# Kernel optimization log

Hardware: AMD Instinct MI355X
Metric: run time of the kernel (lower is better)

Reference implementation:

```python
import jax, jax.numpy as jnp
import numpy as np

B, T, N, FIN = 32, 12, 1024, 64
K, OUT_F = 3, 64


def setup_inputs() -> dict:
    key = jax.random.key(0)
    k1, k2, k3 = jax.random.split(key, 3)
    x = jax.random.normal(k1, (B, T, N, FIN), dtype=jnp.float32)
    A = jax.random.uniform(k2, (B, N, N), dtype=jnp.float32)
    # Xavier-uniform-like init for Theta [K, in_f, out_f]
    limit = float(np.sqrt(6.0 / (FIN + OUT_F)))
    Theta = jax.random.uniform(k3, (K, FIN, OUT_F), dtype=jnp.float32,
                               minval=-limit, maxval=limit)
    return {"x": x, "A": A, "Theta": Theta}


def reference(x, A, Theta):
    Bb, Tt, Nn, Fin = x.shape
    Kk = Theta.shape[0]
    I = jnp.broadcast_to(jnp.eye(Nn, dtype=x.dtype), (Bb, Nn, Nn))
    # lambda_max = max row-sum of A, clamped to >= 1
    lambda_max = jnp.maximum(jnp.max(jnp.sum(A, axis=-1), axis=-1), 1.0)
    L = 2.0 * A / lambda_max[:, None, None] - I  # scaled Laplacian surrogate [B,N,N]
    out = jnp.zeros((Bb, Tt, Nn, Theta.shape[-1]), dtype=x.dtype)
    T_prev2, T_prev = None, I
    for k in range(Kk):  # small fixed K-hop loop
        if k == 0:
            T_k = I
        elif k == 1:
            T_k = L
        else:
            T_k = 2.0 * jnp.einsum('bnm,bmp->bnp', L, T_prev) - T_prev2
        T_prev2, T_prev = T_prev, T_k
        rhs = jnp.einsum('btnf,fo->btno', x, Theta[k])   # feature transform
        out = out + jnp.einsum('bnm,btmo->btno', T_k, rhs)  # graph aggregation
    return jax.nn.relu(out)
```

## Files before the change

kernel.cpp:

```cpp
#include <hip/hip_runtime.h>

typedef unsigned short ushort_t;
typedef unsigned char uchar_t;
typedef __attribute__((ext_vector_type(8))) __bf16 bf16x8;
typedef __attribute__((ext_vector_type(4))) float f32x4;
typedef __attribute__((ext_vector_type(8))) unsigned short u16x8;
typedef __attribute__((ext_vector_type(8))) int i32x8;

#define NB 32
#define TT 12
#define NNODE 1024
#define FF 64
#define OO 64
#define TO 768

#define SCL_ONE 127
#define SCL_E   118

__device__ __forceinline__ unsigned short f2bf(float f) {
    unsigned u = __float_as_uint(f);
    u += 0x7FFFu + ((u >> 16) & 1u);
    return (unsigned short)(u >> 16);
}
__device__ __forceinline__ float bf2f(unsigned short h) {
    return __uint_as_float(((unsigned)h) << 16);
}
__device__ __forceinline__ unsigned char f2fp8(float f) {
    return (unsigned char)(__builtin_amdgcn_cvt_pk_fp8_f32(f, f, 0, false) & 0xff);
}

__device__ __forceinline__ void gload16(const void* g, void* l) {
    __builtin_amdgcn_global_load_lds(
        (const __attribute__((address_space(1))) unsigned int*)g,
        (__attribute__((address_space(3))) unsigned int*)l, 16, 0, 0);
}

__global__ void k_init(unsigned* lam) {
    if (threadIdx.x < NB) lam[threadIdx.x] = 0x3F800000u;
}

__global__ __launch_bounds__(256) void k_rowmax(const float* __restrict__ A,
                                                unsigned* __restrict__ lam) {
    const int b = blockIdx.x >> 4;
    const int chunk = blockIdx.x & 15;
    const int w = threadIdx.x >> 6, lane = threadIdx.x & 63;
    const float* Ab = A + (size_t)b * NNODE * NNODE;
    float mx = 0.0f;
    for (int r = 0; r < 16; ++r) {
        const float* rp = Ab + (size_t)(chunk * 64 + w * 16 + r) * NNODE;
        float s = 0.0f;
#pragma unroll
        for (int j = 0; j < 16; ++j) s += rp[lane + j * 64];
#pragma unroll
        for (int off = 32; off > 0; off >>= 1) s += __shfl_down(s, off, 64);
        if (lane == 0) mx = fmaxf(mx, s);
    }
    if (lane == 0) atomicMax(&lam[b], __float_as_uint(mx));
}

__global__ __launch_bounds__(256) void k_escale(const float* __restrict__ A,
                                                const unsigned* __restrict__ lam,
                                                uchar_t* __restrict__ E8) {
    const size_t idx = ((size_t)blockIdx.x * 256 + threadIdx.x) * 8;
    const int b = (int)(idx >> 20);
    const float scl = 1024.0f / __uint_as_float(lam[b]);
    const float4 v0 = *(const float4*)(A + idx);
    const float4 v1 = *(const float4*)(A + idx + 4);
    unsigned lo = 0, hi = 0;
    lo = (unsigned)__builtin_amdgcn_cvt_pk_fp8_f32(v0.x * scl, v0.y * scl, (int)lo, false);
    lo = (unsigned)__builtin_amdgcn_cvt_pk_fp8_f32(v0.z * scl, v0.w * scl, (int)lo, true);
    hi = (unsigned)__builtin_amdgcn_cvt_pk_fp8_f32(v1.x * scl, v1.y * scl, (int)hi, false);
    hi = (unsigned)__builtin_amdgcn_cvt_pk_fp8_f32(v1.z * scl, v1.w * scl, (int)hi, true);
    uint2 pk; pk.x = lo; pk.y = hi;
    *(uint2*)(E8 + idx) = pk;
}

__global__ void k_theta(const float* __restrict__ Th, ushort_t* __restrict__ Tht) {
    int tid = blockIdx.x * 256 + threadIdx.x;
    if (tid < 3 * 64 * 64) {
        int k = tid >> 12, rem = tid & 4095, o = rem >> 6, f = rem & 63;
        Tht[tid] = f2bf(Th[(k << 12) + (f << 6) + o]);
    }
}

__global__ __launch_bounds__(512, 5) void k_feature(const float* __restrict__ x,
                                                    const ushort_t* __restrict__ Tht,
                                                    ushort_t* __restrict__ Pb,
                                                    ushort_t* __restrict__ Qc,
                                                    uchar_t* __restrict__ R2f8) {
    __shared__ __align__(16) uchar_t th[3 * 64 * 128];
    __shared__ __align__(16) uchar_t tbuf[26624];
    ushort_t* tbq = (ushort_t*)tbuf;
    char* tbr = (char*)(tbuf + 17408);

    const int n0 = blockIdx.x * 128;
    const int t = blockIdx.y;
    const int b = blockIdx.z;
    const int tid = threadIdx.x;
    const int w = tid >> 6, lane = tid & 63, quad = lane >> 4, l15 = lane & 15;

#pragma unroll
    for (int i = 0; i < 3; ++i) {
        int chunk = i * 512 + tid;
        int ko = chunk >> 3, c = chunk & 7;
        int phys = c ^ (ko & 7);
        const int4 v = *(const int4*)(Tht + ko * 64 + c * 8);
        *(int4*)(th + ko * 128 + phys * 16) = v;
    }

    const float* xr = x + (((size_t)b * TT + t) * NNODE + n0 + w * 16 + l15) * FF;
    bf16x8 af[2];
#pragma unroll
    for (int ks = 0; ks < 2; ++ks) {
        const float4 v0 = *(const float4*)(xr + ks * 32 + quad * 8);
        const float4 v1 = *(const float4*)(xr + ks * 32 + quad * 8 + 4);
        u16x8 p;
        p[0] = f2bf(v0.x); p[1] = f2bf(v0.y); p[2] = f2bf(v0.z); p[3] = f2bf(v0.w);
        p[4] = f2bf(v1.x); p[5] = f2bf(v1.y); p[6] = f2bf(v1.z); p[7] = f2bf(v1.w);
        af[ks] = *(bf16x8*)&p;
    }
    __syncthreads();

    f32x4 acc[3][4];
#pragma unroll
    for (int k = 0; k < 3; ++k)
#pragma unroll
        for (int cb = 0; cb < 4; ++cb) acc[k][cb] = (f32x4){0.f, 0.f, 0.f, 0.f};

#pragma unroll
    for (int k = 0; k < 3; ++k)
#pragma unroll
        for (int ks = 0; ks < 2; ++ks)
#pragma unroll
            for (int cb = 0; cb < 4; ++cb) {
                const int o = cb * 16 + l15;
                const int c = (ks * 4 + quad) ^ (o & 7);
                const bf16x8 bfr = *(const bf16x8*)(th + (k * 64 + o) * 128 + c * 16);
                acc[k][cb] = __builtin_amdgcn_mfma_f32_16x16x32_bf16(af[ks], bfr, acc[k][cb], 0, 0, 0);
            }

    ushort_t* Pbb = Pb + (((size_t)b * TT + t) * NNODE + n0) * OO;
#pragma unroll
    for (int cb = 0; cb < 4; ++cb)
#pragma unroll
        for (int r = 0; r < 4; ++r) {
            const int n = w * 16 + quad * 4 + r;
            const int o = cb * 16 + l15;
            Pbb[(size_t)n * OO + o] = f2bf(acc[0][cb][r] - acc[2][cb][r]);
        }

#pragma unroll
    for (int cb = 0; cb < 4; ++cb)
#pragma unroll
        for (int r = 0; r < 4; ++r) {
            const int nl = w * 16 + quad * 4 + r;
            const int o = cb * 16 + l15;
            tbq[o * 136 + nl] = f2bf(acc[1][cb][r] - 2.0f * acc[2][cb][r]);
            tbr[o * 144 + nl] = (char)f2fp8(acc[2][cb][r]);
        }
    __syncthreads();

    {
        const int o = tid >> 3, seg = tid & 7;
        ushort_t* qrow = Qc + ((size_t)b * TO + t * 64 + o) * NNODE + n0 + seg * 16;
        const ushort_t* sq = tbq + o * 136 + seg * 16;
        *(u16x8*)(qrow) = *(const u16x8*)(sq);
        *(u16x8*)(qrow + 8) = *(const u16x8*)(sq + 8);
        uchar_t* rrow = R2f8 + ((size_t)b * TO + t * 64 + o) * NNODE + n0 + seg * 16;
        *(int4*)rrow = *(const int4*)(tbr + o * 144 + seg * 16);
    }
}

template <int MODE>
__global__ __launch_bounds__(256, 3) void k_gemm8(const uchar_t* __restrict__ Aop, size_t aBS,
                                                  const uchar_t* __restrict__ Bop, size_t bBS,
                                                  const ushort_t* __restrict__ Qc,
                                                  uchar_t* __restrict__ Zf8,
                                                  ushort_t* __restrict__ Pbp,
                                                  float* __restrict__ outp) {
    __shared__ __align__(16) uchar_t smem[49152];
    const int bid = blockIdx.x;
    const int xcd = bid & 7, y = bid >> 3;
    const int tile = y % 48;
    const int b = xcd + 8 * (y / 48);
    const int tm = (MODE == 1) ? (tile >> 3) : (tile / 6);
    const int tn = (MODE == 1) ? (tile & 7) : (tile % 6);
    const int m0 = tm * 128, n0 = tn * 128;
    const int tid = threadIdx.x;
    const int w = tid >> 6, lane = tid & 63, quad = lane >> 4, l15 = lane & 15;
    const int wr = w >> 1, wc = w & 1;
    const uchar_t* Ab = Aop + (size_t)b * aBS + (size_t)m0 * NNODE;
    const uchar_t* Bb = Bop + (size_t)b * bBS + (size_t)n0 * NNODE;

    int ldso[4];
    size_t goff[4];
#pragma unroll
    for (int i = 0; i < 4; ++i) {
        int slot = i * 256 + tid;
        int row = slot >> 3;
        int lc = (slot & 7) ^ (row & 7);
        ldso[i] = slot * 16;
        goff[i] = (size_t)row * NNODE + lc * 16;
    }

    f32x4 acc[4][4];
#pragma unroll
    for (int i = 0; i < 4; ++i)
#pragma unroll
        for (int j = 0; j < 4; ++j) acc[i][j] = (f32x4){0.f, 0.f, 0.f, 0.f};

#pragma unroll
    for (int i = 0; i < 4; ++i) gload16(Ab + goff[i], smem + ldso[i]);
#pragma unroll
    for (int i = 0; i < 4; ++i) gload16(Bb + goff[i], smem + 16384 + ldso[i]);

#pragma unroll
    for (int kk = 0; kk < 8; ++kk) {
        const uchar_t* At = smem;
        const uchar_t* Bt = smem + 16384 + ((kk & 1) << 14);
        uchar_t* Btn = smem + 16384 + (((kk & 1) ^ 1) << 14);
        if (kk < 7) {
            const int k0 = (kk + 1) << 7;
#pragma unroll
            for (int i = 0; i < 4; ++i) gload16(Bb + k0 + goff[i], Btn + ldso[i]);
            asm volatile("s_waitcnt vmcnt(4)" ::: "memory");
        } else {
            asm volatile("s_waitcnt vmcnt(0)" ::: "memory");
        }
        __builtin_amdgcn_s_barrier();

        i32x8 af[4], bfr[4];
#pragma unroll
        for (int i = 0; i < 4; ++i) {
            const int m = wr * 64 + i * 16 + l15;
            const int n = wc * 64 + i * 16 + l15;
            const int4 alo = *(const int4*)(At + m * 128 + (((quad << 1)) ^ (m & 7)) * 16);
            const int4 ahi = *(const int4*)(At + m * 128 + (((quad << 1) | 1) ^ (m & 7)) * 16);
            const int4 blo = *(const int4*)(Bt + n * 128 + (((quad << 1)) ^ (n & 7)) * 16);
            const int4 bhi = *(const int4*)(Bt + n * 128 + (((quad << 1) | 1) ^ (n & 7)) * 16);
            af[i] = (i32x8){alo.x, alo.y, alo.z, alo.w, ahi.x, ahi.y, ahi.z, ahi.w};
            bfr[i] = (i32x8){blo.x, blo.y, blo.z, blo.w, bhi.x, bhi.y, bhi.z, bhi.w};
        }
        asm volatile("s_waitcnt lgkmcnt(0)" ::: "memory");
        __builtin_amdgcn_s_barrier();
        if (kk < 7) {
            const int k0 = (kk + 1) << 7;
#pragma unroll
            for (int i = 0; i < 4; ++i) gload16(Ab + k0 + goff[i], smem + ldso[i]);
        }
        __builtin_amdgcn_s_setprio(1);
#pragma unroll
        for (int i = 0; i < 4; ++i)
#pragma unroll
            for (int j = 0; j < 4; ++j)
                acc[i][j] = __builtin_amdgcn_mfma_scale_f32_16x16x128_f8f6f4(
                    af[i], bfr[j], acc[i][j], 0, 0, 0, SCL_ONE, 0, SCL_E);
        __builtin_amdgcn_s_setprio(0);
    }
    __syncthreads();

    if (MODE == 1) {
        ushort_t* tb = (ushort_t*)smem;
        const ushort_t* Qb = Qc + (size_t)b * TO * NNODE;
        uchar_t* Zb = Zf8 + (size_t)b * TO * NNODE;
#pragma unroll
        for (int i = 0; i < 4; ++i)
#pragma unroll
            for (int r = 0; r < 4; ++r) {
                const int cl = wr * 64 + i * 16 + quad * 4 + r;
                const int c = m0 + cl;
#pragma unroll
                for (int j = 0; j < 4; ++j) {
                    const int nl = wc * 64 + j * 16 + l15;
                    const size_t zi = (size_t)c * NNODE + n0 + nl;
                    const float z = bf2f(Qb[zi]) + 2.0f * acc[i][j][r];
                    Zb[zi] = f2fp8(z);
                    tb[nl * 136 + cl] = f2bf(z);
                }
            }
        __syncthreads();
        const int t0 = m0 >> 6;
        const int row = tid >> 1, half = tid & 1;
        ushort_t* prow = Pbp + (((size_t)b * TT + t0 + half) * NNODE + n0 + row) * OO;
        const ushort_t* srow = tb + row * 136 + half * 64;
#pragma unroll
        for (int s = 0; s < 8; ++s) {
            u16x8 pv = *(const u16x8*)(prow + s * 8);
            u16x8 zv = *(const u16x8*)(srow + s * 8);
            u16x8 rv;
#pragma unroll
            for (int e = 0; e < 8; ++e) rv[e] = f2bf(bf2f(pv[e]) - bf2f(zv[e]));
            *(u16x8*)(prow + s * 8) = rv;
        }
    } else {
#pragma unroll
        for (int i = 0; i < 4; ++i)
#pragma unroll
            for (int r = 0; r < 4; ++r) {
                const int n = m0 + wr * 64 + i * 16 + quad * 4 + r;
#pragma unroll
                for (int j = 0; j < 4; ++j) {
                    const int c = n0 + wc * 64 + j * 16 + l15;
                    const int t = c >> 6, o = c & 63;
                    const size_t id = (((size_t)b * TT + t) * NNODE + n) * OO + o;
                    outp[id] = fmaxf(bf2f(Pbp[id]) + acc[i][j][r], 0.0f);
                }
            }
    }
}

extern "C" void kernel_launch(void* const* d_in, const int* in_sizes, int n_in,
                              void* d_out, int out_size, void* d_ws, size_t ws_size,
                              hipStream_t stream) {
    const float* x = (const float*)d_in[0];
    const float* A = (const float*)d_in[1];
    const float* Th = (const float*)d_in[2];
    float* out = (float*)d_out;
    char* ws = (char*)d_ws;

    unsigned* lam = (unsigned*)ws;
    uchar_t* E8 = (uchar_t*)(ws + 256);
    uchar_t* R2f8 = E8 + (size_t)NB * NNODE * NNODE;
    uchar_t* Zf8 = R2f8 + (size_t)NB * TO * NNODE;
    ushort_t* Qc = (ushort_t*)(Zf8 + (size_t)NB * TO * NNODE);
    ushort_t* Pb = Qc + (size_t)NB * TO * NNODE;
    ushort_t* Tht = Pb + (size_t)NB * TT * NNODE * OO;

    k_init<<<1, 64, 0, stream>>>(lam);
    k_rowmax<<<512, 256, 0, stream>>>(A, lam);
    k_escale<<<16384, 256, 0, stream>>>(A, lam, E8);
    k_theta<<<48, 256, 0, stream>>>(Th, Tht);
    k_feature<<<dim3(8, 12, 32), 512, 0, stream>>>(x, Tht, Pb, Qc, R2f8);
    k_gemm8<1><<<1536, 256, 0, stream>>>(R2f8, (size_t)TO * NNODE,
                                         E8, (size_t)NNODE * NNODE,
                                         Qc, Zf8, Pb, nullptr);
    k_gemm8<2><<<1536, 256, 0, stream>>>(E8, (size_t)NNODE * NNODE,
                                         Zf8, (size_t)TO * NNODE,
                                         nullptr, nullptr, Pb, out);
}
```

Before: 431.9 us.

## Fuse row-sum max into fp8 quantization pass and apply lambda scale in GEMM epilogues

The separate row-max kernel and the A-to-fp8 scaling kernel are merged into one pass over A. A is quantized with a fixed factor of 2, so the conversion no longer depends on lambda_max. Each 256-thread block covers exactly two rows, so it also reduces the row sums and does an atomicMax. The 1/lambda factor is moved into the GEMM epilogues as scalar multipliers, and the MFMA scale for E changes to unity. This removes one full read of the 128MB A matrix, at the cost of different fp8 dynamic range for A (values near 2 rather than normalized), which may affect precision.

```diff
diff --git a/kernel.cpp b/kernel.cpp
--- a/kernel.cpp
+++ b/kernel.cpp
@@ -15,7 +15,6 @@
 #define TO 768
 
 #define SCL_ONE 127
-#define SCL_E   118
 
 __device__ __forceinline__ unsigned short f2bf(float f) {
     unsigned u = __float_as_uint(f);
@@ -39,40 +38,31 @@
     if (threadIdx.x < NB) lam[threadIdx.x] = 0x3F800000u;
 }
 
-__global__ __launch_bounds__(256) void k_rowmax(const float* __restrict__ A,
-                                                unsigned* __restrict__ lam) {
-    const int b = blockIdx.x >> 4;
-    const int chunk = blockIdx.x & 15;
-    const int w = threadIdx.x >> 6, lane = threadIdx.x & 63;
-    const float* Ab = A + (size_t)b * NNODE * NNODE;
-    float mx = 0.0f;
-    for (int r = 0; r < 16; ++r) {
-        const float* rp = Ab + (size_t)(chunk * 64 + w * 16 + r) * NNODE;
-        float s = 0.0f;
-#pragma unroll
-        for (int j = 0; j < 16; ++j) s += rp[lane + j * 64];
-#pragma unroll
-        for (int off = 32; off > 0; off >>= 1) s += __shfl_down(s, off, 64);
-        if (lane == 0) mx = fmaxf(mx, s);
-    }
-    if (lane == 0) atomicMax(&lam[b], __float_as_uint(mx));
-}
-
-__global__ __launch_bounds__(256) void k_escale(const float* __restrict__ A,
-                                                const unsigned* __restrict__ lam,
-                                                uchar_t* __restrict__ E8) {
+__global__ __launch_bounds__(256) void k_prep(const float* __restrict__ A,
+                                              unsigned* __restrict__ lam,
+                                              uchar_t* __restrict__ E8) {
+    __shared__ float ls[4];
     const size_t idx = ((size_t)blockIdx.x * 256 + threadIdx.x) * 8;
     const int b = (int)(idx >> 20);
-    const float scl = 1024.0f / __uint_as_float(lam[b]);
     const float4 v0 = *(const float4*)(A + idx);
     const float4 v1 = *(const float4*)(A + idx + 4);
     unsigned lo = 0, hi = 0;
-    lo = (unsigned)__builtin_amdgcn_cvt_pk_fp8_f32(v0.x * scl, v0.y * scl, (int)lo, false);
-    lo = (unsigned)__builtin_amdgcn_cvt_pk_fp8_f32(v0.z * scl, v0.w * scl, (int)lo, true);
-    hi = (unsigned)__builtin_amdgcn_cvt_pk_fp8_f32(v1.x * scl, v1.y * scl, (int)hi, false);
-    hi = (unsigned)__builtin_amdgcn_cvt_pk_fp8_f32(v1.z * scl, v1.w * scl, (int)hi, true);
+    lo = (unsigned)__builtin_amdgcn_cvt_pk_fp8_f32(v0.x * 2.0f, v0.y * 2.0f, (int)lo, false);
+    lo = (unsigned)__builtin_amdgcn_cvt_pk_fp8_f32(v0.z * 2.0f, v0.w * 2.0f, (int)lo, true);
+    hi = (unsigned)__builtin_amdgcn_cvt_pk_fp8_f32(v1.x * 2.0f, v1.y * 2.0f, (int)hi, false);
+    hi = (unsigned)__builtin_amdgcn_cvt_pk_fp8_f32(v1.z * 2.0f, v1.w * 2.0f, (int)hi, true);
     uint2 pk; pk.x = lo; pk.y = hi;
     *(uint2*)(E8 + idx) = pk;
+    float s = v0.x + v0.y + v0.z + v0.w + v1.x + v1.y + v1.z + v1.w;
+#pragma unroll
+    for (int off = 32; off > 0; off >>= 1) s += __shfl_down(s, off, 64);
+    const int w = threadIdx.x >> 6;
+    if ((threadIdx.x & 63) == 0) ls[w] = s;
+    __syncthreads();
+    if (threadIdx.x == 0) {
+        const float r0 = ls[0] + ls[1], r1 = ls[2] + ls[3];
+        atomicMax(&lam[b], __float_as_uint(fmaxf(r0, r1)));
+    }
 }
 
 __global__ void k_theta(const float* __restrict__ Th, ushort_t* __restrict__ Tht) {
@@ -174,6 +164,7 @@
 template <int MODE>
 __global__ __launch_bounds__(256, 3) void k_gemm8(const uchar_t* __restrict__ Aop, size_t aBS,
                                                   const uchar_t* __restrict__ Bop, size_t bBS,
+                                                  const unsigned* __restrict__ lam,
                                                   const ushort_t* __restrict__ Qc,
                                                   uchar_t* __restrict__ Zf8,
                                                   ushort_t* __restrict__ Pbp,
@@ -191,6 +182,7 @@
     const int wr = w >> 1, wc = w & 1;
     const uchar_t* Ab = Aop + (size_t)b * aBS + (size_t)m0 * NNODE;
     const uchar_t* Bb = Bop + (size_t)b * bBS + (size_t)n0 * NNODE;
+    const float lamf = __uint_as_float(lam[b]);
 
     int ldso[4];
     size_t goff[4];
@@ -254,12 +246,13 @@
 #pragma unroll
             for (int j = 0; j < 4; ++j)
                 acc[i][j] = __builtin_amdgcn_mfma_scale_f32_16x16x128_f8f6f4(
-                    af[i], bfr[j], acc[i][j], 0, 0, 0, SCL_ONE, 0, SCL_E);
+                    af[i], bfr[j], acc[i][j], 0, 0, 0, SCL_ONE, 0, SCL_ONE);
         __builtin_amdgcn_s_setprio(0);
     }
     __syncthreads();
 
     if (MODE == 1) {
+        const float c1 = 2.0f / lamf;
         ushort_t* tb = (ushort_t*)smem;
         const ushort_t* Qb = Qc + (size_t)b * TO * NNODE;
         uchar_t* Zb = Zf8 + (size_t)b * TO * NNODE;
@@ -273,7 +266,7 @@
                 for (int j = 0; j < 4; ++j) {
                     const int nl = wc * 64 + j * 16 + l15;
                     const size_t zi = (size_t)c * NNODE + n0 + nl;
-                    const float z = bf2f(Qb[zi]) + 2.0f * acc[i][j][r];
+                    const float z = bf2f(Qb[zi]) + c1 * acc[i][j][r];
                     Zb[zi] = f2fp8(z);
                     tb[nl * 136 + cl] = f2bf(z);
                 }
@@ -293,6 +286,7 @@
             *(u16x8*)(prow + s * 8) = rv;
         }
     } else {
+        const float c2 = 1.0f / lamf;
 #pragma unroll
         for (int i = 0; i < 4; ++i)
 #pragma unroll
@@ -303,7 +297,7 @@
                     const int c = n0 + wc * 64 + j * 16 + l15;
                     const int t = c >> 6, o = c & 63;
                     const size_t id = (((size_t)b * TT + t) * NNODE + n) * OO + o;
-                    outp[id] = fmaxf(bf2f(Pbp[id]) + acc[i][j][r], 0.0f);
+                    outp[id] = fmaxf(bf2f(Pbp[id]) + c2 * acc[i][j][r], 0.0f);
                 }
             }
     }
@@ -327,14 +321,13 @@
     ushort_t* Tht = Pb + (size_t)NB * TT * NNODE * OO;
 
     k_init<<<1, 64, 0, stream>>>(lam);
-    k_rowmax<<<512, 256, 0, stream>>>(A, lam);
-    k_escale<<<16384, 256, 0, stream>>>(A, lam, E8);
+    k_prep<<<16384, 256, 0, stream>>>(A, lam, E8);
     k_theta<<<48, 256, 0, stream>>>(Th, Tht);
     k_feature<<<dim3(8, 12, 32), 512, 0, stream>>>(x, Tht, Pb, Qc, R2f8);
     k_gemm8<1><<<1536, 256, 0, stream>>>(R2f8, (size_t)TO * NNODE,
                                          E8, (size_t)NNODE * NNODE,
-                                         Qc, Zf8, Pb, nullptr);
+                                         lam, Qc, Zf8, Pb, nullptr);
     k_gemm8<2><<<1536, 256, 0, stream>>>(E8, (size_t)NNODE * NNODE,
                                          Zf8, (size_t)TO * NNODE,
-                                         nullptr, nullptr, Pb, out);
-}
+                                         lam, nullptr, nullptr, Pb, out);
+}
```

New measurement: 500.1 us. 1.16x slower.
